# Optimization experiments

Measured on AMD Instinct MI355X. Metric: run time of the kernel, lower is better.

The kernel has to match this reference:

```python
import jax, jax.numpy as jnp
import numpy as np

SHAPE = (32, 32, 32768)  # (struct_dim, struct_dim, Z dense values axis)


def setup_inputs() -> dict:
    key = jax.random.key(0)
    k0, k1, k2 = jax.random.split(key, 3)
    x0 = jax.random.normal(k0, SHAPE, dtype=jnp.float32)  # used as (b, c, Z)
    x1 = jax.random.normal(k1, SHAPE, dtype=jnp.float32)  # used as (a, b, Z)
    x2 = jax.random.normal(k2, SHAPE, dtype=jnp.float32)  # used as (c, d, Z)
    return {"x0": x0, "x1": x1, "x2": x2}


def reference(x0, x1, x2):
    # einnet.forward with cmd = [('abZ,bcZ->acZ',(0,1)), ('acZ,cdZ->adZ',(0,1))].
    # For positions (0,1) the module passes operands in reversed order, so:
    # step 1: einsum('abZ,bcZ->acZ', x1, x0)   -> y1 (a, c, Z)
    # step 2: einsum('acZ,cdZ->adZ', y1, x2)   -> y2 (a, d, Z)
    # The 'Z' axis is the dense values axis of the COO tensors: each op is a
    # batch of Z independent 32x32 matmuls. Dense einsum is mathematically
    # identical to the sparse COO filter/match/coalesce path.
    y1 = jnp.einsum('abZ,bcZ->acZ', x1, x0)
    y2 = jnp.einsum('acZ,cdZ->adZ', y1, x2)
    return y2
```

## Files before the change

### kernel.cpp

```cpp
#include <hip/hip_runtime.h>

#define Z_TOTAL 32768
#define ZC 32
#define THREADS 256

__global__ __launch_bounds__(THREADS, 3) void einnet_kernel(
    const float* __restrict__ x0,
    const float* __restrict__ x1,
    const float* __restrict__ x2,
    float* __restrict__ out)
{
    __shared__ float lds[8192];

    const int tid = threadIdx.x;
    const int bid = blockIdx.x;
    const int zc    = (bid >> 4) * 8 + (bid & 7);
    const int ahalf = (bid >> 3) & 1;
    const int z0 = zc * ZC;
    const int zl = tid & 31;
    const int ag = tid >> 5;
    const int a0 = ahalf * 16 + ag * 2;

    float y1[2][32];
    float y2[2][32];
    #pragma unroll
    for (int r = 0; r < 2; ++r) {
        #pragma unroll
        for (int c = 0; c < 32; ++c) { y1[r][c] = 0.f; y2[r][c] = 0.f; }
    }

    #pragma unroll 1
    for (int bq = 0; bq < 4; ++bq) {
        float x1q[2][8];
        #pragma unroll
        for (int r = 0; r < 2; ++r) {
            #pragma unroll
            for (int bl = 0; bl < 8; ++bl)
                x1q[r][bl] = x1[(size_t)((a0 + r) * 32 + bq * 8 + bl) * Z_TOTAL + z0 + zl];
        }

        __syncthreads();
        #pragma unroll
        for (int i = 0; i < 8; ++i) {
            int w   = tid + i * THREADS;
            int pc4 = w >> 5;
            int zs  = w & 31;
            const float* g = x0 + (size_t)(bq * 256 + pc4 * 4) * Z_TOTAL + z0 + zs;
            float4 v;
            v.x = g[0];
            v.y = g[(size_t)Z_TOTAL];
            v.z = g[2 * (size_t)Z_TOTAL];
            v.w = g[3 * (size_t)Z_TOTAL];
            *reinterpret_cast<float4*>(&lds[w * 4]) = v;
        }
        __syncthreads();

        #pragma unroll
        for (int bl = 0; bl < 8; ++bl) {
            #pragma unroll
            for (int c4 = 0; c4 < 8; ++c4) {
                float4 s = *reinterpret_cast<const float4*>(&lds[((bl * 8 + c4) * 32 + zl) * 4]);
                #pragma unroll
                for (int r = 0; r < 2; ++r) {
                    y1[r][c4 * 4 + 0] = fmaf(x1q[r][bl], s.x, y1[r][c4 * 4 + 0]);
                    y1[r][c4 * 4 + 1] = fmaf(x1q[r][bl], s.y, y1[r][c4 * 4 + 1]);
                    y1[r][c4 * 4 + 2] = fmaf(x1q[r][bl], s.z, y1[r][c4 * 4 + 2]);
                    y1[r][c4 * 4 + 3] = fmaf(x1q[r][bl], s.w, y1[r][c4 * 4 + 3]);
                }
            }
        }
    }

    #pragma unroll
    for (int cq = 0; cq < 4; ++cq) {
        __syncthreads();
        #pragma unroll
        for (int i = 0; i < 8; ++i) {
            int w   = tid + i * THREADS;
            int pc4 = w >> 5;
            int zs  = w & 31;
            const float* g = x2 + (size_t)(cq * 256 + pc4 * 4) * Z_TOTAL + z0 + zs;
            float4 v;
            v.x = g[0];
            v.y = g[(size_t)Z_TOTAL];
            v.z = g[2 * (size_t)Z_TOTAL];
            v.w = g[3 * (size_t)Z_TOTAL];
            *reinterpret_cast<float4*>(&lds[w * 4]) = v;
        }
        __syncthreads();

        #pragma unroll
        for (int cl8 = 0; cl8 < 8; ++cl8) {
            #pragma unroll
            for (int d4 = 0; d4 < 8; ++d4) {
                float4 s = *reinterpret_cast<const float4*>(&lds[((cl8 * 8 + d4) * 32 + zl) * 4]);
                #pragma unroll
                for (int r = 0; r < 2; ++r) {
                    float w1 = y1[r][cq * 8 + cl8];
                    y2[r][d4 * 4 + 0] = fmaf(w1, s.x, y2[r][d4 * 4 + 0]);
                    y2[r][d4 * 4 + 1] = fmaf(w1, s.y, y2[r][d4 * 4 + 1]);
                    y2[r][d4 * 4 + 2] = fmaf(w1, s.z, y2[r][d4 * 4 + 2]);
                    y2[r][d4 * 4 + 3] = fmaf(w1, s.w, y2[r][d4 * 4 + 3]);
                }
            }
        }
    }

    #pragma unroll
    for (int r = 0; r < 2; ++r) {
        #pragma unroll
        for (int d = 0; d < 32; ++d)
            out[(size_t)((a0 + r) * 32 + d) * Z_TOTAL + z0 + zl] = y2[r][d];
    }
}

extern "C" void kernel_launch(void* const* d_in, const int* in_sizes, int n_in,
                              void* d_out, int out_size, void* d_ws, size_t ws_size,
                              hipStream_t stream) {
    const float* x0 = (const float*)d_in[0];
    const float* x1 = (const float*)d_in[1];
    const float* x2 = (const float*)d_in[2];
    float* out = (float*)d_out;

    dim3 grid(2048);
    dim3 block(THREADS);
    hipLaunchKernelGGL(einnet_kernel, grid, block, 0, stream, x0, x1, x2, out);
}
```

Measured before the change: 179.0 us.

## Double-buffer LDS tiles and prefetch next slab into registers during compute

Splits both matmul stages into eight smaller slabs of 4 rows and double-buffers them in LDS. The next slab of x0/x2 and the next x1 values are loaded into registers before the current slab's FMAs run, then written to the other buffer. This hides global-load latency behind compute and halves the barriers per slab. The cost is extra registers for the prefetch (g, xn) under a launch bound of 3 blocks, which may cause spills or lower occupancy.

```diff
diff --git a/kernel.cpp b/kernel.cpp
--- a/kernel.cpp
+++ b/kernel.cpp
@@ -1,7 +1,7 @@
 #include <hip/hip_runtime.h>
 
 #define Z_TOTAL 32768
-#define ZC 32
+#define ZTL ((size_t)Z_TOTAL)
 #define THREADS 256
 
 __global__ __launch_bounds__(THREADS, 3) void einnet_kernel(
@@ -16,87 +16,107 @@
     const int bid = blockIdx.x;
     const int zc    = (bid >> 4) * 8 + (bid & 7);
     const int ahalf = (bid >> 3) & 1;
-    const int z0 = zc * ZC;
+    const int z0 = zc * 32;
     const int zl = tid & 31;
     const int ag = tid >> 5;
     const int a0 = ahalf * 16 + ag * 2;
 
     float y1[2][32];
-    float y2[2][32];
     #pragma unroll
-    for (int r = 0; r < 2; ++r) {
+    for (int r = 0; r < 2; ++r)
         #pragma unroll
-        for (int c = 0; c < 32; ++c) { y1[r][c] = 0.f; y2[r][c] = 0.f; }
+        for (int c = 0; c < 32; ++c) y1[r][c] = 0.f;
+
+    float4 g[4];
+    float xv[2][4];
+    float xn[2][4];
+
+    #pragma unroll
+    for (int i = 0; i < 4; ++i) {
+        const float* s = x0 + (size_t)(i * 32 + ag * 4) * ZTL + z0 + zl;
+        g[i].x = s[0]; g[i].y = s[ZTL]; g[i].z = s[2 * ZTL]; g[i].w = s[3 * ZTL];
     }
+    #pragma unroll
+    for (int r = 0; r < 2; ++r)
+        #pragma unroll
+        for (int bl = 0; bl < 4; ++bl)
+            xv[r][bl] = x1[(size_t)((a0 + r) * 32 + bl) * ZTL + z0 + zl];
+
+    #pragma unroll
+    for (int i = 0; i < 4; ++i)
+        *reinterpret_cast<float4*>(&lds[((i * 8 + ag) * 32 + zl) * 4]) = g[i];
+    __syncthreads();
 
     #pragma unroll 1
-    for (int bq = 0; bq < 4; ++bq) {
-        float x1q[2][8];
+    for (int t = 0; t < 8; ++t) {
+        const float* nsrc = (t < 7) ? (x0 + (size_t)(t + 1) * 128 * ZTL) : x2;
         #pragma unroll
-        for (int r = 0; r < 2; ++r) {
+        for (int i = 0; i < 4; ++i) {
+            const float* s = nsrc + (size_t)(i * 32 + ag * 4) * ZTL + z0 + zl;
+            g[i].x = s[0]; g[i].y = s[ZTL]; g[i].z = s[2 * ZTL]; g[i].w = s[3 * ZTL];
+        }
+        const int tn = (t + 1) & 7;
+        #pragma unroll
+        for (int r = 0; r < 2; ++r)
             #pragma unroll
-            for (int bl = 0; bl < 8; ++bl)
-                x1q[r][bl] = x1[(size_t)((a0 + r) * 32 + bq * 8 + bl) * Z_TOTAL + z0 + zl];
-        }
+            for (int bl = 0; bl < 4; ++bl)
+                xn[r][bl] = x1[(size_t)((a0 + r) * 32 + tn * 4 + bl) * ZTL + z0 + zl];
 
-        __syncthreads();
+        const float* buf = &lds[(t & 1) * 4096];
         #pragma unroll
-        for (int i = 0; i < 8; ++i) {
-            int w   = tid + i * THREADS;
-            int pc4 = w >> 5;
-            int zs  = w & 31;
-            const float* g = x0 + (size_t)(bq * 256 + pc4 * 4) * Z_TOTAL + z0 + zs;
-            float4 v;
-            v.x = g[0];
-            v.y = g[(size_t)Z_TOTAL];
-            v.z = g[2 * (size_t)Z_TOTAL];
-            v.w = g[3 * (size_t)Z_TOTAL];
-            *reinterpret_cast<float4*>(&lds[w * 4]) = v;
-        }
-        __syncthreads();
-
-        #pragma unroll
-        for (int bl = 0; bl < 8; ++bl) {
+        for (int bl = 0; bl < 4; ++bl) {
             #pragma unroll
             for (int c4 = 0; c4 < 8; ++c4) {
-                float4 s = *reinterpret_cast<const float4*>(&lds[((bl * 8 + c4) * 32 + zl) * 4]);
+                float4 s = *reinterpret_cast<const float4*>(
+                    &buf[((bl * 8 + c4) * 32 + zl) * 4]);
                 #pragma unroll
                 for (int r = 0; r < 2; ++r) {
-                    y1[r][c4 * 4 + 0] = fmaf(x1q[r][bl], s.x, y1[r][c4 * 4 + 0]);
-                    y1[r][c4 * 4 + 1] = fmaf(x1q[r][bl], s.y, y1[r][c4 * 4 + 1]);
-                    y1[r][c4 * 4 + 2] = fmaf(x1q[r][bl], s.z, y1[r][c4 * 4 + 2]);
-                    y1[r][c4 * 4 + 3] = fmaf(x1q[r][bl], s.w, y1[r][c4 * 4 + 3]);
+                    y1[r][c4 * 4 + 0] = fmaf(xv[r][bl], s.x, y1[r][c4 * 4 + 0]);
+                    y1[r][c4 * 4 + 1] = fmaf(xv[r][bl], s.y, y1[r][c4 * 4 + 1]);
+                    y1[r][c4 * 4 + 2] = fmaf(xv[r][bl], s.z, y1[r][c4 * 4 + 2]);
+                    y1[r][c4 * 4 + 3] = fmaf(xv[r][bl], s.w, y1[r][c4 * 4 + 3]);
                 }
             }
         }
+
+        float* wbuf = &lds[((t + 1) & 1) * 4096];
+        #pragma unroll
+        for (int i = 0; i < 4; ++i)
+            *reinterpret_cast<float4*>(&wbuf[((i * 8 + ag) * 32 + zl) * 4]) = g[i];
+        #pragma unroll
+        for (int r = 0; r < 2; ++r)
+            #pragma unroll
+            for (int bl = 0; bl < 4; ++bl) xv[r][bl] = xn[r][bl];
+        __syncthreads();
     }
 
+    float y2[2][32];
     #pragma unroll
-    for (int cq = 0; cq < 4; ++cq) {
-        __syncthreads();
+    for (int r = 0; r < 2; ++r)
         #pragma unroll
-        for (int i = 0; i < 8; ++i) {
-            int w   = tid + i * THREADS;
-            int pc4 = w >> 5;
-            int zs  = w & 31;
-            const float* g = x2 + (size_t)(cq * 256 + pc4 * 4) * Z_TOTAL + z0 + zs;
-            float4 v;
-            v.x = g[0];
-            v.y = g[(size_t)Z_TOTAL];
-            v.z = g[2 * (size_t)Z_TOTAL];
-            v.w = g[3 * (size_t)Z_TOTAL];
-            *reinterpret_cast<float4*>(&lds[w * 4]) = v;
+        for (int d = 0; d < 32; ++d) y2[r][d] = 0.f;
+
+    #pragma unroll
+    for (int t = 0; t < 8; ++t) {
+        if (t < 7) {
+            const float* nsrc = x2 + (size_t)(t + 1) * 128 * ZTL;
+            #pragma unroll
+            for (int i = 0; i < 4; ++i) {
+                const float* s = nsrc + (size_t)(i * 32 + ag * 4) * ZTL + z0 + zl;
+                g[i].x = s[0]; g[i].y = s[ZTL]; g[i].z = s[2 * ZTL]; g[i].w = s[3 * ZTL];
+            }
         }
-        __syncthreads();
 
+        const float* buf = &lds[(t & 1) * 4096];
         #pragma unroll
-        for (int cl8 = 0; cl8 < 8; ++cl8) {
+        for (int cl = 0; cl < 4; ++cl) {
             #pragma unroll
             for (int d4 = 0; d4 < 8; ++d4) {
-                float4 s = *reinterpret_cast<const float4*>(&lds[((cl8 * 8 + d4) * 32 + zl) * 4]);
+                float4 s = *reinterpret_cast<const float4*>(
+                    &buf[((cl * 8 + d4) * 32 + zl) * 4]);
                 #pragma unroll
                 for (int r = 0; r < 2; ++r) {
-                    float w1 = y1[r][cq * 8 + cl8];
+                    const float w1 = y1[r][t * 4 + cl];
                     y2[r][d4 * 4 + 0] = fmaf(w1, s.x, y2[r][d4 * 4 + 0]);
                     y2[r][d4 * 4 + 1] = fmaf(w1, s.y, y2[r][d4 * 4 + 1]);
                     y2[r][d4 * 4 + 2] = fmaf(w1, s.z, y2[r][d4 * 4 + 2]);
@@ -104,13 +124,21 @@
                 }
             }
         }
+
+        if (t < 7) {
+            float* wbuf = &lds[((t + 1) & 1) * 4096];
+            #pragma unroll
+            for (int i = 0; i < 4; ++i)
+                *reinterpret_cast<float4*>(&wbuf[((i * 8 + ag) * 32 + zl) * 4]) = g[i];
+            __syncthreads();
+        }
     }
 
     #pragma unroll
     for (int r = 0; r < 2; ++r) {
         #pragma unroll
         for (int d = 0; d < 32; ++d)
-            out[(size_t)((a0 + r) * 32 + d) * Z_TOTAL + z0 + zl] = y2[r][d];
+            out[(size_t)((a0 + r) * 32 + d) * ZTL + z0 + zl] = y2[r][d];
     }
 }
 
```

Measured after the change: 593.4 us. 3.32x slower.

## Double-buffer operand tiles in LDS via async global_load_lds pipeline

Applied to the files above, without the earlier changes.

Replaces the synchronous register-staged loads of x0/x2 tiles with __builtin_amdgcn_global_load_lds direct-to-LDS copies, double-buffered across a 16-stage pipeline that spans both einsum steps. x1 is now also staged through LDS instead of per-thread global loads, and the next tile's load is issued before waiting on vmcnt, so memory latency overlaps with FMA work. The cost is more LDS per block (48KB) and launch bounds lowered to 2 blocks per CU, which reduces occupancy, plus reliance on hand-tuned waitcnt counts.

```diff
diff --git a/kernel.cpp b/kernel.cpp
--- a/kernel.cpp
+++ b/kernel.cpp
@@ -1,116 +1,142 @@
 #include <hip/hip_runtime.h>
 
-#define Z_TOTAL 32768
-#define ZC 32
+#define ZT 32768
+#define ZTL ((size_t)ZT)
 #define THREADS 256
 
-__global__ __launch_bounds__(THREADS, 3) void einnet_kernel(
+
+#define GLDS(src, dst) __builtin_amdgcn_global_load_lds( \
+    (const __attribute__((address_space(1))) void*)(src), \
+    (__attribute__((address_space(3))) void*)(dst), 4, 0, 0)
+
+__global__ __launch_bounds__(THREADS, 2) void einnet_kernel(
     const float* __restrict__ x0,
     const float* __restrict__ x1,
     const float* __restrict__ x2,
     float* __restrict__ out)
 {
-    __shared__ float lds[8192];
+    __shared__ float lds[12288];
 
-    const int tid = threadIdx.x;
-    const int bid = blockIdx.x;
+    const int tid  = threadIdx.x;
+    const int lane = tid & 63;
+    const int wv   = tid >> 6;
+    const int bid  = blockIdx.x;
     const int zc    = (bid >> 4) * 8 + (bid & 7);
     const int ahalf = (bid >> 3) & 1;
-    const int z0 = zc * ZC;
+    const int z0 = zc * 32;
     const int zl = tid & 31;
     const int ag = tid >> 5;
-    const int a0 = ahalf * 16 + ag * 2;
+
+    const size_t inv0 = (size_t)(lane & 3) * ZTL + (size_t)(lane >> 2);
+    const size_t inv1 = (size_t)(lane >> 5) * ZTL + (size_t)(lane & 31);
+
+    auto stageMain = [&](const float* mat, int tt, float* bb) {
+        const float* mb = mat + (size_t)(tt * 128 + wv * 32) * ZTL + z0 + inv0;
+        float* db = bb + wv * 1024;
+        #pragma unroll
+        for (int i = 0; i < 16; ++i)
+            GLDS(mb + (size_t)((i >> 1) * 4) * ZTL + (i & 1) * 16, db + i * 64);
+    };
+    auto stageX1 = [&](int tt, float* bb) {
+        const float* m1 = x1 + (size_t)((ahalf * 16 + wv * 4) * 32 + tt * 4) * ZTL + z0 + inv1;
+        float* d1 = bb + 4096 + wv * 512;
+        #pragma unroll
+        for (int i = 0; i < 8; ++i)
+            GLDS(m1 + (size_t)((i >> 1) * 32 + (i & 1) * 2) * ZTL, d1 + i * 64);
+    };
 
     float y1[2][32];
+    #pragma unroll
+    for (int r = 0; r < 2; ++r)
+        #pragma unroll
+        for (int c = 0; c < 32; ++c) y1[r][c] = 0.f;
+
+    stageMain(x0, 0, &lds[0]);     stageX1(0, &lds[0]);
+    stageMain(x0, 1, &lds[6144]);  stageX1(1, &lds[6144]);
+    asm volatile("s_waitcnt vmcnt(24)" ::: "memory");
+    __builtin_amdgcn_s_barrier();
+
+    #pragma unroll 1
+    for (int t = 0; t < 8; ++t) {
+        const float* bb  = &lds[(t & 1) * 6144];
+        const float* x1b = bb + 4096;
+        #pragma unroll
+        for (int bl = 0; bl < 4; ++bl) {
+            float xa = x1b[((ag * 2 + 0) * 4 + bl) * 32 + zl];
+            float xb = x1b[((ag * 2 + 1) * 4 + bl) * 32 + zl];
+            #pragma unroll
+            for (int c4 = 0; c4 < 8; ++c4) {
+                float4 s = *reinterpret_cast<const float4*>(
+                    &bb[((bl * 8 + c4) * 32 + zl) * 4]);
+                y1[0][c4 * 4 + 0] = fmaf(xa, s.x, y1[0][c4 * 4 + 0]);
+                y1[0][c4 * 4 + 1] = fmaf(xa, s.y, y1[0][c4 * 4 + 1]);
+                y1[0][c4 * 4 + 2] = fmaf(xa, s.z, y1[0][c4 * 4 + 2]);
+                y1[0][c4 * 4 + 3] = fmaf(xa, s.w, y1[0][c4 * 4 + 3]);
+                y1[1][c4 * 4 + 0] = fmaf(xb, s.x, y1[1][c4 * 4 + 0]);
+                y1[1][c4 * 4 + 1] = fmaf(xb, s.y, y1[1][c4 * 4 + 1]);
+                y1[1][c4 * 4 + 2] = fmaf(xb, s.z, y1[1][c4 * 4 + 2]);
+                y1[1][c4 * 4 + 3] = fmaf(xb, s.w, y1[1][c4 * 4 + 3]);
+            }
+        }
+
+        asm volatile("" ::: "memory");
+        __builtin_amdgcn_s_barrier();
+
+        const int s = t + 2;
+        float* nb = &lds[(s & 1) * 6144];
+        if (s < 8) { stageMain(x0, s, nb); stageX1(s, nb); }
+        else       { stageMain(x2, s - 8, nb); }
+        if (t < 6) asm volatile("s_waitcnt vmcnt(24)" ::: "memory");
+        else       asm volatile("s_waitcnt vmcnt(16)" ::: "memory");
+        __builtin_amdgcn_s_barrier();
+    }
+
     float y2[2][32];
     #pragma unroll
-    for (int r = 0; r < 2; ++r) {
+    for (int r = 0; r < 2; ++r)
         #pragma unroll
-        for (int c = 0; c < 32; ++c) { y1[r][c] = 0.f; y2[r][c] = 0.f; }
-    }
+        for (int d = 0; d < 32; ++d) y2[r][d] = 0.f;
 
-    #pragma unroll 1
-    for (int bq = 0; bq < 4; ++bq) {
-        float x1q[2][8];
+    #pragma unroll
+    for (int u = 0; u < 8; ++u) {
+        const float* bb = &lds[(u & 1) * 6144];
         #pragma unroll
-        for (int r = 0; r < 2; ++r) {
+        for (int cl = 0; cl < 4; ++cl) {
+            const float wa = y1[0][u * 4 + cl];
+            const float wb = y1[1][u * 4 + cl];
             #pragma unroll
-            for (int bl = 0; bl < 8; ++bl)
-                x1q[r][bl] = x1[(size_t)((a0 + r) * 32 + bq * 8 + bl) * Z_TOTAL + z0 + zl];
+            for (int d4 = 0; d4 < 8; ++d4) {
+                float4 s = *reinterpret_cast<const float4*>(
+                    &bb[((cl * 8 + d4) * 32 + zl) * 4]);
+                y2[0][d4 * 4 + 0] = fmaf(wa, s.x, y2[0][d4 * 4 + 0]);
+                y2[0][d4 * 4 + 1] = fmaf(wa, s.y, y2[0][d4 * 4 + 1]);
+                y2[0][d4 * 4 + 2] = fmaf(wa, s.z, y2[0][d4 * 4 + 2]);
+                y2[0][d4 * 4 + 3] = fmaf(wa, s.w, y2[0][d4 * 4 + 3]);
+                y2[1][d4 * 4 + 0] = fmaf(wb, s.x, y2[1][d4 * 4 + 0]);
+                y2[1][d4 * 4 + 1] = fmaf(wb, s.y, y2[1][d4 * 4 + 1]);
+                y2[1][d4 * 4 + 2] = fmaf(wb, s.z, y2[1][d4 * 4 + 2]);
+                y2[1][d4 * 4 + 3] = fmaf(wb, s.w, y2[1][d4 * 4 + 3]);
+            }
         }
 
-        __syncthreads();
-        #pragma unroll
-        for (int i = 0; i < 8; ++i) {
-            int w   = tid + i * THREADS;
-            int pc4 = w >> 5;
-            int zs  = w & 31;
-            const float* g = x0 + (size_t)(bq * 256 + pc4 * 4) * Z_TOTAL + z0 + zs;
-            float4 v;
-            v.x = g[0];
-            v.y = g[(size_t)Z_TOTAL];
-            v.z = g[2 * (size_t)Z_TOTAL];
-            v.w = g[3 * (size_t)Z_TOTAL];
-            *reinterpret_cast<float4*>(&lds[w * 4]) = v;
-        }
-        __syncthreads();
-
-        #pragma unroll
-        for (int bl = 0; bl < 8; ++bl) {
-            #pragma unroll
-            for (int c4 = 0; c4 < 8; ++c4) {
-                float4 s = *reinterpret_cast<const float4*>(&lds[((bl * 8 + c4) * 32 + zl) * 4]);
-                #pragma unroll
-                for (int r = 0; r < 2; ++r) {
-                    y1[r][c4 * 4 + 0] = fmaf(x1q[r][bl], s.x, y1[r][c4 * 4 + 0]);
-                    y1[r][c4 * 4 + 1] = fmaf(x1q[r][bl], s.y, y1[r][c4 * 4 + 1]);
-                    y1[r][c4 * 4 + 2] = fmaf(x1q[r][bl], s.z, y1[r][c4 * 4 + 2]);
-                    y1[r][c4 * 4 + 3] = fmaf(x1q[r][bl], s.w, y1[r][c4 * 4 + 3]);
-                }
-            }
+        asm volatile("" ::: "memory");
+        if (u < 6) {
+            __builtin_amdgcn_s_barrier();
+            stageMain(x2, u + 2, &lds[(u & 1) * 6144]);
+            asm volatile("s_waitcnt vmcnt(16)" ::: "memory");
+            __builtin_amdgcn_s_barrier();
+        } else if (u == 6) {
+            asm volatile("s_waitcnt vmcnt(0)" ::: "memory");
+            __builtin_amdgcn_s_barrier();
         }
     }
 
-    #pragma unroll
-    for (int cq = 0; cq < 4; ++cq) {
-        __syncthreads();
-        #pragma unroll
-        for (int i = 0; i < 8; ++i) {
-            int w   = tid + i * THREADS;
-            int pc4 = w >> 5;
-            int zs  = w & 31;
-            const float* g = x2 + (size_t)(cq * 256 + pc4 * 4) * Z_TOTAL + z0 + zs;
-            float4 v;
-            v.x = g[0];
-            v.y = g[(size_t)Z_TOTAL];
-            v.z = g[2 * (size_t)Z_TOTAL];
-            v.w = g[3 * (size_t)Z_TOTAL];
-            *reinterpret_cast<float4*>(&lds[w * 4]) = v;
-        }
-        __syncthreads();
-
-        #pragma unroll
-        for (int cl8 = 0; cl8 < 8; ++cl8) {
-            #pragma unroll
-            for (int d4 = 0; d4 < 8; ++d4) {
-                float4 s = *reinterpret_cast<const float4*>(&lds[((cl8 * 8 + d4) * 32 + zl) * 4]);
-                #pragma unroll
-                for (int r = 0; r < 2; ++r) {
-                    float w1 = y1[r][cq * 8 + cl8];
-                    y2[r][d4 * 4 + 0] = fmaf(w1, s.x, y2[r][d4 * 4 + 0]);
-                    y2[r][d4 * 4 + 1] = fmaf(w1, s.y, y2[r][d4 * 4 + 1]);
-                    y2[r][d4 * 4 + 2] = fmaf(w1, s.z, y2[r][d4 * 4 + 2]);
-                    y2[r][d4 * 4 + 3] = fmaf(w1, s.w, y2[r][d4 * 4 + 3]);
-                }
-            }
-        }
-    }
-
+    const int a0 = ahalf * 16 + ag * 2;
     #pragma unroll
     for (int r = 0; r < 2; ++r) {
         #pragma unroll
         for (int d = 0; d < 32; ++d)
-            out[(size_t)((a0 + r) * 32 + d) * Z_TOTAL + z0 + zl] = y2[r][d];
+            out[(size_t)((a0 + r) * 32 + d) * ZTL + z0 + zl] = y2[r][d];
     }
 }
 
```

Result: slower. 485.9 us (+171.5%).
